# Kernel optimization log

Hardware: AMD Instinct MI355X
Metric: run time of the kernel (lower is better)

The kernel has to match this reference:

```python
import jax, jax.numpy as jnp
import numpy as np

B, K = 16, 50
IN_CH, N_CLASSES, N_ANCH = 256, 80, 3
STRIDE, FSIZE, IGNORE_THRE = 8, 76, 0.7
N_CH = 5 + N_CLASSES
ANCHORS = np.array([[10,13],[16,30],[33,23],[30,61],[62,45],[59,119],[116,90],[156,198],[373,326]], np.float32)
ALL_GRID = ANCHORS / STRIDE            # all 9 anchors in grid units
ANCH_MASK = np.array([0, 1, 2])        # layer_no = 2
MASKED = ALL_GRID[ANCH_MASK]           # (3,2) anchors used by this head


def setup_inputs():
    key = jax.random.key(0)
    k1, k2, k3, k4, k5, k6 = jax.random.split(key, 6)
    xin = jax.random.normal(k1, (B, IN_CH, FSIZE, FSIZE), jnp.float32)
    cls = jax.random.randint(k2, (B, K), 0, N_CLASSES).astype(jnp.float32)
    xy = jax.random.uniform(k3, (B, K, 2), minval=0.05, maxval=0.95)
    wh = jax.random.uniform(k4, (B, K, 2), minval=0.02, maxval=0.30)
    labels = jnp.concatenate([cls[..., None], xy, wh], -1)   # (B,K,5) [cls,xc,yc,w,h]
    oc = N_ANCH * N_CH
    conv_w = jax.random.normal(k5, (oc, IN_CH), jnp.float32) * 0.01
    conv_b = jax.random.normal(k6, (oc,), jnp.float32) * 0.01
    return {"xin": xin, "labels": labels, "conv_w": conv_w, "conv_b": conv_b}


def _yolo(xin, conv_w, conv_b, labels):
    f, C = FSIZE, N_CLASSES
    # 1x1 conv == channel matmul
    raw = jnp.einsum('bchw,oc->bohw', xin, conv_w) + conv_b[None, :, None, None]
    raw = raw.reshape(B, N_ANCH, N_CH, f, f).transpose(0, 1, 3, 4, 2)  # (B,A,f,f,85)
    # sigmoid on x,y,obj,cls; w,h stay raw
    out = jnp.concatenate([jax.nn.sigmoid(raw[..., :2]), raw[..., 2:4], jax.nn.sigmoid(raw[..., 4:])], -1)

    grid = jnp.arange(f, dtype=jnp.float32)
    mw = jnp.asarray(MASKED[:, 0]); mh = jnp.asarray(MASKED[:, 1])
    px = out[..., 0] + grid[None, None, None, :]
    py = out[..., 1] + grid[None, None, :, None]
    pw = jnp.exp(out[..., 2]) * mw[None, :, None, None]
    ph = jnp.exp(out[..., 3]) * mh[None, :, None, None]
    pred = jax.lax.stop_gradient(jnp.stack([px, py, pw, ph], -1))  # detached, like torch .data

    labels = jax.lax.stop_gradient(labels)
    valid = labels.sum(-1) > 0                  # (B,K) padding rows are all-zero
    tx = labels[..., 1] * f; ty = labels[..., 2] * f
    tw = labels[..., 3] * f; th = labels[..., 4] * f
    ii = tx.astype(jnp.int32); jj = ty.astype(jnp.int32)

    # anchor matching: IoU of [0,0,w,h] truth vs [0,0,aw,ah] ref anchors (corners at origin)
    aw = jnp.asarray(ALL_GRID[:, 0]); ah = jnp.asarray(ALL_GRID[:, 1])
    inter_a = jnp.minimum(tw[..., None], aw) * jnp.minimum(th[..., None], ah)  # (B,K,9)
    iou_a = inter_a / (tw[..., None] * th[..., None] + aw * ah - inter_a)
    best_n_all = jnp.argmax(iou_a, -1)
    best_n = best_n_all % 3
    best_mask = (best_n_all == ANCH_MASK[0]) | (best_n_all == ANCH_MASK[1]) | (best_n_all == ANCH_MASK[2])

    # pred-vs-truth IoU in cxcywh form (xyxy=False)
    pa = pred.reshape(B, -1, 4)                 # (B, A*f*f, 4)
    tb = jnp.stack([tx, ty, tw, th], -1)        # (B, K, 4)
    tl = jnp.maximum(pa[:, :, None, :2] - pa[:, :, None, 2:] * 0.5, tb[:, None, :, :2] - tb[:, None, :, 2:] * 0.5)
    br = jnp.minimum(pa[:, :, None, :2] + pa[:, :, None, 2:] * 0.5, tb[:, None, :, :2] + tb[:, None, :, 2:] * 0.5)
    en = jnp.all(tl < br, -1)
    inter = jnp.prod(br - tl, -1) * en
    area_p = pa[..., 2] * pa[..., 3]; area_t = tb[..., 2] * tb[..., 3]
    iou_p = inter / (area_p[:, :, None] + area_t[:, None, :] - inter)
    iou_p = jnp.where(valid[:, None, :], iou_p, 0.0)
    ignore = (iou_p.max(-1) > IGNORE_THRE).reshape(B, N_ANCH, f, f)
    obj_mask = 1.0 - ignore.astype(jnp.float32)

    # scatter positive targets; non-selected rows routed out-of-bounds and dropped
    sel = valid & best_mask
    bb = jnp.where(sel, jnp.arange(B)[:, None], B)
    obj_mask = obj_mask.at[bb, best_n, jj, ii].set(1.0, mode='drop')
    tgt_mask = jnp.zeros((B, N_ANCH, f, f, 4 + C)).at[bb, best_n, jj, ii].set(1.0, mode='drop')
    scale = jnp.sqrt(2.0 - tw * th / (f * f))
    tgt_scale = jnp.zeros((B, N_ANCH, f, f, 2)).at[bb, best_n, jj, ii].set(
        jnp.broadcast_to(scale[..., None], (B, K, 2)), mode='drop')
    tvals = jnp.concatenate([
        (tx - ii)[..., None], (ty - jj)[..., None],
        jnp.log(tw / mw[best_n] + 1e-16)[..., None],
        jnp.log(th / mh[best_n] + 1e-16)[..., None],
        jnp.ones((B, K, 1), jnp.float32),
        jax.nn.one_hot(labels[..., 0].astype(jnp.int32), C)], -1)  # (B,K,85)
    target = jnp.zeros((B, N_ANCH, f, f, N_CH)).at[bb, best_n, jj, ii].set(tvals, mode='drop')

    oxy = out[..., :2] * tgt_mask[..., :2]
    owh = out[..., 2:4] * tgt_mask[..., 2:4] * tgt_scale
    oob = out[..., 4] * obj_mask
    ocl = out[..., 5:] * tgt_mask[..., 4:]
    txy = target[..., :2] * tgt_mask[..., :2]
    twh = target[..., 2:4] * tgt_mask[..., 2:4] * tgt_scale
    tob = target[..., 4] * obj_mask
    tcl = target[..., 5:] * tgt_mask[..., 4:]

    def bce(p, t, w=None):
        pc = jnp.clip(p, 1e-12, 1.0 - 1e-7)
        e = -(t * jnp.log(pc) + (1.0 - t) * jnp.log(1.0 - pc))
        if w is not None:
            e = e * w
        return e.sum()

    loss_xy = bce(oxy, txy, tgt_scale * tgt_scale)
    loss_wh = 0.5 * jnp.sum((owh - twh) ** 2)
    loss_obj = bce(oob, tob)
    loss_cls = bce(ocl, tcl)
    out_m = jnp.concatenate([oxy, owh, oob[..., None], ocl], -1)
    tgt_m = jnp.concatenate([txy, twh, tob[..., None], tcl], -1)
    loss_l2 = jnp.sum((out_m - tgt_m) ** 2)
    loss = loss_xy + loss_wh + loss_obj + loss_cls
    return loss, loss_xy, loss_wh, loss_obj, loss_cls, loss_l2, out_m


def reference(xin, labels, conv_w, conv_b):
    return _yolo(xin, conv_w, conv_b, labels)
```

## Files before the change

kernel.cpp:

```cpp
#include <hip/hip_runtime.h>
#include <hip/hip_bf16.h>

#define B_   16
#define K_   50
#define CIN  256
#define F_   76
#define A_   3
#define NCH  85
#define OC   255
#define HW   (F_*F_)
#define SLAB (F_*NCH)

#define WS_BIAS_F 0
#define WS_LAB_F  256
#define WS_W15P_F 13056
#define WS_B15_F  17152
#define WS_CNT_F  17168
#define WS_REC_F  17184
#define WS_PART_F 23584
#define WS_OMV_F  35872
#define WS_END_F  313120

#define NTL   46
#define NCONV (B_*NTL)
#define NREC  800
#define NROW  (NCONV + NREC)

__device__ __constant__ float AW9[9] = {1.25f, 2.0f, 4.125f, 3.75f, 7.75f, 7.375f, 14.5f, 19.5f, 46.625f};
__device__ __constant__ float AH9[9] = {1.625f, 3.75f, 2.875f, 7.625f, 5.625f, 14.875f, 11.25f, 24.75f, 40.75f};

__device__ __forceinline__ float sigm(float r) { return 1.0f / (1.0f + __expf(-r)); }
__device__ __forceinline__ float bce_t(float p, float tv) {
    float pc = fminf(fmaxf(p, 1e-12f), 1.0f - 1e-7f);
    return -(tv * __logf(pc) + (1.0f - tv) * __logf(1.0f - pc));
}

__global__ void prep_kernel(const float* __restrict__ conv_w, const float* __restrict__ conv_b,
                            const float* __restrict__ labels, float* __restrict__ ws) {
    int bid = blockIdx.x, t = threadIdx.x;
    if (bid == 0) {
        ws[WS_BIAS_F + t] = (t < OC) ? conv_b[t] : 0.0f;
    } else if (bid == 1) {
        for (int idx = t; idx < B_ * K_; idx += 256) {
            const float* L = labels + idx * 5;
            float cls = L[0], xc = L[1], yc = L[2], wl = L[3], hl = L[4];
            float ssum = cls + xc + yc + wl + hl;
            float validf = (ssum > 0.0f) ? 1.0f : 0.0f;
            float tx = xc * F_, ty = yc * F_, tw = wl * F_, th = hl * F_;
            int ii = (int)tx, jj = (int)ty;
            float tarea = tw * th;
            float best = -1.0f; int bn = 0;
            #pragma unroll
            for (int n = 0; n < 9; n++) {
                float inter = fminf(tw, AW9[n]) * fminf(th, AH9[n]);
                float iou = inter / (tarea + AW9[n] * AH9[n] - inter);
                if (iou > best) { best = iou; bn = n; }
            }
            int a = bn % 3;
            bool self = (validf != 0.0f) && (bn < 3);
            float* R = ws + WS_LAB_F + idx * 16;
            R[0] = tx; R[1] = ty; R[2] = tw; R[3] = th;
            R[4] = validf; R[5] = self ? (float)a : -1.0f; R[6] = (float)ii; R[7] = (float)jj;
            R[8] = tx - (float)ii; R[9] = ty - (float)jj;
            R[10] = __logf(tw / AW9[a] + 1e-16f);
            R[11] = __logf(th / AH9[a] + 1e-16f);
            R[12] = sqrtf(2.0f - tarea / (float)HW);
            R[13] = cls; R[14] = 0.0f; R[15] = 0.0f;
        }
    } else {
        for (int idx = t; idx < 4096; idx += 256) {
            int c = idx >> 4, r = idx & 15;
            float v = 0.0f;
            if (r < 15) v = conv_w[((r / 5) * NCH + (r % 5)) * CIN + c];
            ws[WS_W15P_F + idx] = v;
        }
        if (t < 16) ws[WS_B15_F + t] = (t < 15) ? conv_b[(t / 5) * NCH + (t % 5)] : 0.0f;
        if (t == 16) *(int*)(ws + WS_CNT_F) = 0;
    }
}

__global__ __launch_bounds__(256) void convloss_kernel(const float* __restrict__ xin,
                                                       float* __restrict__ ws) {
    __shared__ float4 LAB[K_ * 4];
    __shared__ float accS[128][16];
    __shared__ float redS[2][4];

    const int t = threadIdx.x;
    const int blk = blockIdx.x;
    const int b = blk / NTL, tile = blk - b * NTL;
    const int ph = t & 127;
    const int p0 = tile * 128 + ph;
    const bool ok = p0 < HW;
    const int p = ok ? p0 : HW - 1;
    const int half = __builtin_amdgcn_readfirstlane(t) >> 7;

    if (t < K_ * 4) LAB[t] = ((const float4*)(ws + WS_LAB_F + b * (K_ * 16)))[t];

    const float* xp = xin + (size_t)b * CIN * HW + (size_t)half * 128 * HW + p;
    const float* Wp = ws + WS_W15P_F + half * 128 * 16;

    float acc[15];
    #pragma unroll
    for (int r = 0; r < 15; r++) acc[r] = 0.0f;

    float xv[8];
    #pragma unroll
    for (int u = 0; u < 8; u++) xv[u] = xp[(size_t)u * HW];
    #pragma unroll 1
    for (int c8 = 0; c8 < 16; c8++) {
        float xn[8];
        const int cnx = (c8 < 15) ? (c8 + 1) : 15;
        #pragma unroll
        for (int u = 0; u < 8; u++) xn[u] = xp[(size_t)(cnx * 8 + u) * HW];
        #pragma unroll
        for (int u = 0; u < 8; u++) {
            const float xvu = xv[u];
            const float* wrow = Wp + (c8 * 8 + u) * 16;
            #pragma unroll
            for (int r = 0; r < 15; r++) acc[r] = fmaf(xvu, wrow[r], acc[r]);
        }
        #pragma unroll
        for (int u = 0; u < 8; u++) xv[u] = xn[u];
    }

    if (half) {
        #pragma unroll
        for (int r = 0; r < 15; r++) accS[ph][r] = acc[r];
    }
    __syncthreads();

    float lxy = 0.0f, lwh = 0.0f, lobj = 0.0f, l2 = 0.0f;
    if (t < 128 && ok) {
        #pragma unroll
        for (int r = 0; r < 15; r++) acc[r] += accS[ph][r] + ws[WS_B15_F + r];
        const int j = p / F_, i = p - j * F_;
        const float fi_t = (float)i, fj_t = (float)j;
        float X[3], Y[3], WR[3], HR[3], OB[3], HPW[3], HPH[3], ARP[3], PX[3], PY[3];
        #pragma unroll
        for (int a = 0; a < 3; a++) {
            X[a] = sigm(acc[a * 5 + 0]); Y[a] = sigm(acc[a * 5 + 1]);
            WR[a] = acc[a * 5 + 2]; HR[a] = acc[a * 5 + 3]; OB[a] = sigm(acc[a * 5 + 4]);
            PX[a] = X[a] + fi_t; PY[a] = Y[a] + fj_t;
            float pw = __expf(WR[a]) * AW9[a], phh = __expf(HR[a]) * AH9[a];
            HPW[a] = pw * 0.5f; HPH[a] = phh * 0.5f; ARP[a] = pw * phh;
        }
        float mxi[3] = {0.0f, 0.0f, 0.0f}; int mk[3] = {-1, -1, -1};
        #pragma unroll 2
        for (int k = 0; k < K_; k++) {
            float4 A0 = LAB[4 * k], A1 = LAB[4 * k + 1];
            float tx = A0.x, ty = A0.y, tw = A0.z, th = A0.w;
            float tlx0 = tx - tw * 0.5f, tly0 = ty - th * 0.5f;
            float brx0 = tx + tw * 0.5f, bry0 = ty + th * 0.5f;
            float ta = tw * th, va = A1.x;
            #pragma unroll
            for (int a = 0; a < 3; a++) {
                float tlx = fmaxf(PX[a] - HPW[a], tlx0);
                float tly = fmaxf(PY[a] - HPH[a], tly0);
                float brx = fminf(PX[a] + HPW[a], brx0);
                float bry = fminf(PY[a] + HPH[a], bry0);
                float iw = brx - tlx, ih = bry - tly;
                float inter = (iw > 0.0f && ih > 0.0f) ? iw * ih : 0.0f;
                float iou = __fdividef(inter, ARP[a] + ta - inter);
                iou = (va != 0.0f) ? iou : 0.0f;
                mxi[a] = fmaxf(mxi[a], iou);
                bool match = (A1.y == (float)a) & (A1.z == fi_t) & (A1.w == fj_t);
                mk[a] = match ? k : mk[a];
            }
        }
        #pragma unroll
        for (int a = 0; a < 3; a++) {
            float objmask = (mxi[a] > 0.7f) ? 0.0f : 1.0f;
            float omv;
            if (mk[a] >= 0) {
                float4 B0 = LAB[4 * mk[a] + 2];
                float4 B1 = LAB[4 * mk[a] + 3];
                float sc = B1.x, sc2 = sc * sc;
                lxy += (bce_t(X[a], B0.x) + bce_t(Y[a], B0.y)) * sc2;
                float dw = WR[a] - B0.z, dh = HR[a] - B0.w;
                lwh += 0.5f * sc2 * (dw * dw + dh * dh);
                float pco = fminf(fmaxf(OB[a], 1e-12f), 1.0f - 1e-7f);
                lobj += -__logf(pco);
                float dx = X[a] - B0.x, dy = Y[a] - B0.y, dob = OB[a] - 1.0f;
                l2 += dx * dx + dy * dy + sc2 * (dw * dw + dh * dh) + dob * dob;
                omv = OB[a];
                int ridx = atomicAdd((int*)(ws + WS_CNT_F), 1);
                float* R = ws + WS_REC_F + ridx * 8;
                R[0] = (float)b; R[1] = (float)a; R[2] = (float)p; R[3] = (float)mk[a];
                R[4] = X[a]; R[5] = Y[a]; R[6] = WR[a] * sc; R[7] = HR[a] * sc;
            } else {
                float oo = OB[a] * objmask;
                if (objmask != 0.0f) {
                    float pco = fminf(OB[a], 1.0f - 1e-7f);
                    lobj += -__logf(1.0f - pco);
                }
                l2 += oo * oo;
                omv = oo;
            }
            ws[WS_OMV_F + (size_t)(b * A_ + a) * HW + p] = omv;
        }
    }

    #pragma unroll
    for (int off = 32; off > 0; off >>= 1) {
        lxy += __shfl_down(lxy, off); lwh += __shfl_down(lwh, off);
        lobj += __shfl_down(lobj, off); l2 += __shfl_down(l2, off);
    }
    if (t < 128 && (t & 63) == 0) {
        redS[t >> 6][0] = lxy; redS[t >> 6][1] = lwh;
        redS[t >> 6][2] = lobj; redS[t >> 6][3] = l2;
    }
    __syncthreads();
    if (t == 0) {
        float* P = ws + WS_PART_F + (size_t)blk * 8;
        P[0] = redS[0][0] + redS[1][0];
        P[1] = redS[0][1] + redS[1][1];
        P[2] = redS[0][2] + redS[1][2];
        P[3] = 0.0f;
        P[4] = redS[0][3] + redS[1][3];
    }
}

__global__ __launch_bounds__(256) void writer_kernel(const float* __restrict__ ws,
                                                     float* __restrict__ d_out) {
    const int t = threadIdx.x;
    const int s = blockIdx.x;
    const int baj = s / F_, j = s - baj * F_;
    const float* om = ws + WS_OMV_F + (size_t)baj * HW + j * F_;
    float* slab = d_out + 6 + (size_t)s * SLAB;
    if (t == 0) { slab[0] = 0.0f; slab[1] = 0.0f; slab[6458] = 0.0f; slab[6459] = 0.0f; }
    float4* dst4 = (float4*)(slab + 2);
    for (int n = t; n < 1614; n += 256) {
        int f0 = 2 + 4 * n;
        int p = f0 / 85, r = f0 - 85 * p;
        float4 v = make_float4(0.0f, 0.0f, 0.0f, 0.0f);
        if (r >= 1 && r <= 4) ((float*)&v)[4 - r] = om[p];
        dst4[n] = v;
    }
}

__global__ __launch_bounds__(256) void sparse_kernel(const float* __restrict__ xin,
                                                     const float* __restrict__ conv_w,
                                                     float* __restrict__ ws,
                                                     float* __restrict__ d_out) {
    __shared__ float xcolS[256];
    __shared__ float rr[4][2];
    const int t = threadIdx.x;
    const int idx = blockIdx.x;
    float* P = ws + WS_PART_F + (size_t)(NCONV + idx) * 8;
    const int cnt = *(const int*)(ws + WS_CNT_F);
    if (idx >= cnt) { if (t < 8) P[t] = 0.0f; return; }
    const float* R = ws + WS_REC_F + idx * 8;
    const int b = (int)R[0], a = (int)R[1], p = (int)R[2], k = (int)R[3];
    const int j = p / F_, i = p - j * F_;
    xcolS[t] = xin[((size_t)b * CIN + t) * HW + p];
    __syncthreads();
    const float* Lr = ws + WS_LAB_F + (b * K_ + k) * 16;
    const int cl = (int)Lr[13];
    float* cell = d_out + 6 + (size_t)((b * A_ + a) * F_ + j) * SLAB + i * NCH;
    float lcls = 0.0f, l2 = 0.0f;
    if (t < 80) {
        const int o = a * NCH + 5 + t;
        const float4* wr4 = (const float4*)(conv_w + (size_t)o * CIN);
        float a0 = 0, a1 = 0, a2 = 0, a3 = 0;
        #pragma unroll 8
        for (int q = 0; q < 64; q++) {
            float4 wv = wr4[q];
            a0 = fmaf(wv.x, xcolS[q * 4 + 0], a0);
            a1 = fmaf(wv.y, xcolS[q * 4 + 1], a1);
            a2 = fmaf(wv.z, xcolS[q * 4 + 2], a2);
            a3 = fmaf(wv.w, xcolS[q * 4 + 3], a3);
        }
        float accv = ws[WS_BIAS_F + o] + ((a0 + a1) + (a2 + a3));
        float pc = sigm(accv);
        float tcv = (t == cl) ? 1.0f : 0.0f;
        lcls = bce_t(pc, tcv);
        float d = pc - tcv; l2 = d * d;
        cell[5 + t] = pc;
    } else if (t < 84) {
        cell[t - 80] = R[4 + (t - 80)];
    }
    #pragma unroll
    for (int off = 32; off > 0; off >>= 1) {
        lcls += __shfl_down(lcls, off); l2 += __shfl_down(l2, off);
    }
    if ((t & 63) == 0) { rr[t >> 6][0] = lcls; rr[t >> 6][1] = l2; }
    __syncthreads();
    if (t == 0) {
        P[0] = 0.0f; P[1] = 0.0f; P[2] = 0.0f;
        P[3] = rr[0][0] + rr[1][0] + rr[2][0] + rr[3][0];
        P[4] = rr[0][1] + rr[1][1] + rr[2][1] + rr[3][1];
    }
}

__global__ void finish_kernel(const float* __restrict__ ws, float* __restrict__ d_out) {
    int t = threadIdx.x;
    const float* part = ws + WS_PART_F;
    float s0 = 0, s1 = 0, s2 = 0, s3 = 0, s4 = 0;
    for (int bidx = t; bidx < NROW; bidx += 256) {
        const float* P = part + (size_t)bidx * 8;
        s0 += P[0]; s1 += P[1]; s2 += P[2]; s3 += P[3]; s4 += P[4];
    }
    #pragma unroll
    for (int off = 32; off > 0; off >>= 1) {
        s0 += __shfl_down(s0, off); s1 += __shfl_down(s1, off);
        s2 += __shfl_down(s2, off); s3 += __shfl_down(s3, off);
        s4 += __shfl_down(s4, off);
    }
    __shared__ float red[4][5];
    if ((t & 63) == 0) {
        int w = t >> 6;
        red[w][0] = s0; red[w][1] = s1; red[w][2] = s2; red[w][3] = s3; red[w][4] = s4;
    }
    __syncthreads();
    if (t == 0) {
        float r0 = red[0][0] + red[1][0] + red[2][0] + red[3][0];
        float r1 = red[0][1] + red[1][1] + red[2][1] + red[3][1];
        float r2 = red[0][2] + red[1][2] + red[2][2] + red[3][2];
        float r3 = red[0][3] + red[1][3] + red[2][3] + red[3][3];
        float r4 = red[0][4] + red[1][4] + red[2][4] + red[3][4];
        d_out[0] = r0 + r1 + r2 + r3;
        d_out[1] = r0; d_out[2] = r1; d_out[3] = r2; d_out[4] = r3; d_out[5] = r4;
    }
}

extern "C" void kernel_launch(void* const* d_in, const int* in_sizes, int n_in,
                              void* d_out, int out_size, void* d_ws, size_t ws_size,
                              hipStream_t stream) {
    const float* xin    = (const float*)d_in[0];
    const float* labels = (const float*)d_in[1];
    const float* conv_w = (const float*)d_in[2];
    const float* conv_b = (const float*)d_in[3];
    float* out = (float*)d_out;
    float* ws  = (float*)d_ws;

    prep_kernel<<<3, 256, 0, stream>>>(conv_w, conv_b, labels, ws);
    convloss_kernel<<<NCONV, 256, 0, stream>>>(xin, ws);
    writer_kernel<<<B_ * A_ * F_, 256, 0, stream>>>(ws, out);
    sparse_kernel<<<NREC, 256, 0, stream>>>(xin, conv_w, ws, out);
    finish_kernel<<<1, 256, 0, stream>>>(ws, out);
}
```

Baseline: 224.7 us.

## Split conv channels four ways and parallelize loss epilogue across anchors

```diff
diff --git a/kernel.cpp b/kernel.cpp
--- a/kernel.cpp
+++ b/kernel.cpp
@@ -79,25 +79,24 @@
     }
 }
 
-__global__ __launch_bounds__(256) void convloss_kernel(const float* __restrict__ xin,
+__global__ __launch_bounds__(512) void convloss_kernel(const float* __restrict__ xin,
                                                        float* __restrict__ ws) {
     __shared__ float4 LAB[K_ * 4];
-    __shared__ float accS[128][16];
-    __shared__ float redS[2][4];
+    __shared__ float accS[4][128][17];
+    __shared__ float redS[8][4];
 
     const int t = threadIdx.x;
     const int blk = blockIdx.x;
     const int b = blk / NTL, tile = blk - b * NTL;
     const int ph = t & 127;
+    const int q  = t >> 7;
     const int p0 = tile * 128 + ph;
-    const bool ok = p0 < HW;
-    const int p = ok ? p0 : HW - 1;
-    const int half = __builtin_amdgcn_readfirstlane(t) >> 7;
+    const int p = (p0 < HW) ? p0 : HW - 1;
 
     if (t < K_ * 4) LAB[t] = ((const float4*)(ws + WS_LAB_F + b * (K_ * 16)))[t];
 
-    const float* xp = xin + (size_t)b * CIN * HW + (size_t)half * 128 * HW + p;
-    const float* Wp = ws + WS_W15P_F + half * 128 * 16;
+    const float* xp = xin + (size_t)b * CIN * HW + (size_t)q * 64 * HW + p;
+    const float* Wp = ws + WS_W15P_F + q * 64 * 16;
 
     float acc[15];
     #pragma unroll
@@ -107,9 +106,9 @@
     #pragma unroll
     for (int u = 0; u < 8; u++) xv[u] = xp[(size_t)u * HW];
     #pragma unroll 1
-    for (int c8 = 0; c8 < 16; c8++) {
+    for (int c8 = 0; c8 < 8; c8++) {
         float xn[8];
-        const int cnx = (c8 < 15) ? (c8 + 1) : 15;
+        const int cnx = (c8 < 7) ? (c8 + 1) : 7;
         #pragma unroll
         for (int u = 0; u < 8; u++) xn[u] = xp[(size_t)(cnx * 8 + u) * HW];
         #pragma unroll
@@ -123,80 +122,74 @@
         for (int u = 0; u < 8; u++) xv[u] = xn[u];
     }
 
-    if (half) {
-        #pragma unroll
-        for (int r = 0; r < 15; r++) accS[ph][r] = acc[r];
-    }
+    #pragma unroll
+    for (int r = 0; r < 15; r++) accS[q][ph][r] = acc[r];
     __syncthreads();
 
     float lxy = 0.0f, lwh = 0.0f, lobj = 0.0f, l2 = 0.0f;
-    if (t < 128 && ok) {
-        #pragma unroll
-        for (int r = 0; r < 15; r++) acc[r] += accS[ph][r] + ws[WS_B15_F + r];
-        const int j = p / F_, i = p - j * F_;
-        const float fi_t = (float)i, fj_t = (float)j;
-        float X[3], Y[3], WR[3], HR[3], OB[3], HPW[3], HPH[3], ARP[3], PX[3], PY[3];
-        #pragma unroll
-        for (int a = 0; a < 3; a++) {
-            X[a] = sigm(acc[a * 5 + 0]); Y[a] = sigm(acc[a * 5 + 1]);
-            WR[a] = acc[a * 5 + 2]; HR[a] = acc[a * 5 + 3]; OB[a] = sigm(acc[a * 5 + 4]);
-            PX[a] = X[a] + fi_t; PY[a] = Y[a] + fj_t;
-            float pw = __expf(WR[a]) * AW9[a], phh = __expf(HR[a]) * AH9[a];
-            HPW[a] = pw * 0.5f; HPH[a] = phh * 0.5f; ARP[a] = pw * phh;
-        }
-        float mxi[3] = {0.0f, 0.0f, 0.0f}; int mk[3] = {-1, -1, -1};
-        #pragma unroll 2
-        for (int k = 0; k < K_; k++) {
-            float4 A0 = LAB[4 * k], A1 = LAB[4 * k + 1];
-            float tx = A0.x, ty = A0.y, tw = A0.z, th = A0.w;
-            float tlx0 = tx - tw * 0.5f, tly0 = ty - th * 0.5f;
-            float brx0 = tx + tw * 0.5f, bry0 = ty + th * 0.5f;
-            float ta = tw * th, va = A1.x;
+    if (t < 384) {
+        const int a = t >> 7, pp = t & 127;
+        const int pc = tile * 128 + pp;
+        if (pc < HW) {
+            float c5[5];
             #pragma unroll
-            for (int a = 0; a < 3; a++) {
-                float tlx = fmaxf(PX[a] - HPW[a], tlx0);
-                float tly = fmaxf(PY[a] - HPH[a], tly0);
-                float brx = fminf(PX[a] + HPW[a], brx0);
-                float bry = fminf(PY[a] + HPH[a], bry0);
+            for (int r = 0; r < 5; r++)
+                c5[r] = accS[0][pp][a * 5 + r] + accS[1][pp][a * 5 + r]
+                      + accS[2][pp][a * 5 + r] + accS[3][pp][a * 5 + r]
+                      + ws[WS_B15_F + a * 5 + r];
+            const int j = pc / F_, i = pc - j * F_;
+            const float fi_t = (float)i, fj_t = (float)j, fa_t = (float)a;
+            const float X = sigm(c5[0]), Y = sigm(c5[1]);
+            const float WR = c5[2], HR = c5[3], OB = sigm(c5[4]);
+            const float PX = X + fi_t, PY = Y + fj_t;
+            const float pw_ = __expf(WR) * AW9[a], ph_ = __expf(HR) * AH9[a];
+            const float hpw = pw_ * 0.5f, hph = ph_ * 0.5f, arp = pw_ * ph_;
+
+            float maxiou = 0.0f; int mk = -1;
+            #pragma unroll 2
+            for (int k = 0; k < K_; k++) {
+                float4 A0 = LAB[4 * k], A1 = LAB[4 * k + 1];
+                float tx = A0.x, ty = A0.y, tw = A0.z, th = A0.w;
+                float tlx = fmaxf(PX - hpw, tx - tw * 0.5f);
+                float tly = fmaxf(PY - hph, ty - th * 0.5f);
+                float brx = fminf(PX + hpw, tx + tw * 0.5f);
+                float bry = fminf(PY + hph, ty + th * 0.5f);
                 float iw = brx - tlx, ih = bry - tly;
                 float inter = (iw > 0.0f && ih > 0.0f) ? iw * ih : 0.0f;
-                float iou = __fdividef(inter, ARP[a] + ta - inter);
-                iou = (va != 0.0f) ? iou : 0.0f;
-                mxi[a] = fmaxf(mxi[a], iou);
-                bool match = (A1.y == (float)a) & (A1.z == fi_t) & (A1.w == fj_t);
-                mk[a] = match ? k : mk[a];
+                float iou = __fdividef(inter, arp + tw * th - inter);
+                iou = (A1.x != 0.0f) ? iou : 0.0f;
+                maxiou = fmaxf(maxiou, iou);
+                bool match = (A1.y == fa_t) & (A1.z == fi_t) & (A1.w == fj_t);
+                mk = match ? k : mk;
             }
-        }
-        #pragma unroll
-        for (int a = 0; a < 3; a++) {
-            float objmask = (mxi[a] > 0.7f) ? 0.0f : 1.0f;
+            float objmask = (maxiou > 0.7f) ? 0.0f : 1.0f;
             float omv;
-            if (mk[a] >= 0) {
-                float4 B0 = LAB[4 * mk[a] + 2];
-                float4 B1 = LAB[4 * mk[a] + 3];
+            if (mk >= 0) {
+                float4 B0 = LAB[4 * mk + 2];
+                float4 B1 = LAB[4 * mk + 3];
                 float sc = B1.x, sc2 = sc * sc;
-                lxy += (bce_t(X[a], B0.x) + bce_t(Y[a], B0.y)) * sc2;
-                float dw = WR[a] - B0.z, dh = HR[a] - B0.w;
-                lwh += 0.5f * sc2 * (dw * dw + dh * dh);
-                float pco = fminf(fmaxf(OB[a], 1e-12f), 1.0f - 1e-7f);
-                lobj += -__logf(pco);
-                float dx = X[a] - B0.x, dy = Y[a] - B0.y, dob = OB[a] - 1.0f;
-                l2 += dx * dx + dy * dy + sc2 * (dw * dw + dh * dh) + dob * dob;
-                omv = OB[a];
+                lxy = (bce_t(X, B0.x) + bce_t(Y, B0.y)) * sc2;
+                float dw = WR - B0.z, dh = HR - B0.w;
+                lwh = 0.5f * sc2 * (dw * dw + dh * dh);
+                float pco = fminf(fmaxf(OB, 1e-12f), 1.0f - 1e-7f);
+                lobj = -__logf(pco);
+                float dx = X - B0.x, dy = Y - B0.y, dob = OB - 1.0f;
+                l2 = dx * dx + dy * dy + sc2 * (dw * dw + dh * dh) + dob * dob;
+                omv = OB;
                 int ridx = atomicAdd((int*)(ws + WS_CNT_F), 1);
                 float* R = ws + WS_REC_F + ridx * 8;
-                R[0] = (float)b; R[1] = (float)a; R[2] = (float)p; R[3] = (float)mk[a];
-                R[4] = X[a]; R[5] = Y[a]; R[6] = WR[a] * sc; R[7] = HR[a] * sc;
+                R[0] = (float)b; R[1] = fa_t; R[2] = (float)pc; R[3] = (float)mk;
+                R[4] = X; R[5] = Y; R[6] = WR * sc; R[7] = HR * sc;
             } else {
-                float oo = OB[a] * objmask;
+                float oo = OB * objmask;
                 if (objmask != 0.0f) {
-                    float pco = fminf(OB[a], 1.0f - 1e-7f);
-                    lobj += -__logf(1.0f - pco);
+                    float pco = fminf(OB, 1.0f - 1e-7f);
+                    lobj = -__logf(1.0f - pco);
                 }
-                l2 += oo * oo;
+                l2 = oo * oo;
                 omv = oo;
             }
-            ws[WS_OMV_F + (size_t)(b * A_ + a) * HW + p] = omv;
+            ws[WS_OMV_F + (size_t)(b * A_ + a) * HW + pc] = omv;
         }
     }
 
@@ -205,18 +198,19 @@
         lxy += __shfl_down(lxy, off); lwh += __shfl_down(lwh, off);
         lobj += __shfl_down(lobj, off); l2 += __shfl_down(l2, off);
     }
-    if (t < 128 && (t & 63) == 0) {
+    if ((t & 63) == 0) {
         redS[t >> 6][0] = lxy; redS[t >> 6][1] = lwh;
         redS[t >> 6][2] = lobj; redS[t >> 6][3] = l2;
     }
     __syncthreads();
     if (t == 0) {
+        float s0 = 0, s1 = 0, s2 = 0, s3 = 0;
+        #pragma unroll
+        for (int wv = 0; wv < 8; wv++) {
+            s0 += redS[wv][0]; s1 += redS[wv][1]; s2 += redS[wv][2]; s3 += redS[wv][3];
+        }
         float* P = ws + WS_PART_F + (size_t)blk * 8;
-        P[0] = redS[0][0] + redS[1][0];
-        P[1] = redS[0][1] + redS[1][1];
-        P[2] = redS[0][2] + redS[1][2];
-        P[3] = 0.0f;
-        P[4] = redS[0][3] + redS[1][3];
+        P[0] = s0; P[1] = s1; P[2] = s2; P[3] = 0.0f; P[4] = s3;
     }
 }
 
@@ -334,7 +328,7 @@
     float* ws  = (float*)d_ws;
 
     prep_kernel<<<3, 256, 0, stream>>>(conv_w, conv_b, labels, ws);
-    convloss_kernel<<<NCONV, 256, 0, stream>>>(xin, ws);
+    convloss_kernel<<<NCONV, 512, 0, stream>>>(xin, ws);
     writer_kernel<<<B_ * A_ * F_, 256, 0, stream>>>(ws, out);
     sparse_kernel<<<NREC, 256, 0, stream>>>(xin, conv_w, ws, out);
     finish_kernel<<<1, 256, 0, stream>>>(ws, out);
```

Result: slower. 258.2 us (+14.9%).
